# Performance work log

Measured on AMD Instinct MI355X. Metric: run time of the kernel, lower is better.

The kernel has to match this reference:

```python
import jax, jax.numpy as jnp
import numpy as np

N_NODES = 100000


def setup_inputs() -> dict:
    key = jax.random.key(0)
    ks = jax.random.split(key, 8)
    IN, HID, OUT = 128, 128, 64
    E = 1600000
    x = jax.random.normal(ks[0], (N_NODES, IN), dtype=jnp.float32)
    edge_index = jax.random.randint(ks[1], (2, E), 0, N_NODES, dtype=jnp.int64)
    # PyG SAGEConv params: lin_l (applied to aggregated neighbors, with bias),
    # lin_r (root weight, no bias).
    def lin(k, fi, fo):
        return jax.random.normal(k, (fi, fo), dtype=jnp.float32) / np.sqrt(fi)
    Wl0 = lin(ks[2], IN, HID)
    bl0 = jnp.zeros((HID,), dtype=jnp.float32)
    Wr0 = lin(ks[3], IN, HID)
    Wl1 = lin(ks[4], HID, OUT)
    bl1 = jnp.zeros((OUT,), dtype=jnp.float32)
    Wr1 = lin(ks[5], HID, OUT)
    return {"x": x, "edge_index": edge_index,
            "Wl0": Wl0, "bl0": bl0, "Wr0": Wr0,
            "Wl1": Wl1, "bl1": bl1, "Wr1": Wr1}


def _sage_conv(h, src, dst, Wl, bl, Wr):
    # mean aggregation of source features onto target nodes
    summed = jax.ops.segment_sum(h[src], dst, num_segments=N_NODES)  # [N, d]
    cnt = jax.ops.segment_sum(jnp.ones((src.shape[0], 1), h.dtype), dst,
                              num_segments=N_NODES)                  # [N, 1]
    agg = summed / jnp.maximum(cnt, 1.0)
    return agg @ Wl + bl + h @ Wr


def reference(x, edge_index, Wl0, bl0, Wr0, Wl1, bl1, Wr1):
    src, dst = edge_index[0], edge_index[1]
    h = jax.nn.relu(_sage_conv(x, src, dst, Wl0, bl0, Wr0))
    # dropout is identity in eval mode (training=False)
    return _sage_conv(h, src, dst, Wl1, bl1, Wr1)
```

## Files before the change

### kernel.cpp

```cpp
#include <hip/hip_runtime.h>


typedef short short8 __attribute__((ext_vector_type(8)));
typedef float f32x4 __attribute__((ext_vector_type(4)));
typedef float f32x2 __attribute__((ext_vector_type(2)));

#define NBUCK 782
#define BCAP  3072
#define EPB   8192

static __device__ __forceinline__ unsigned short f2bf(float f) {
    union { float f; unsigned u; } c; c.f = f;
    unsigned u = c.u + 0x7fffu + ((c.u >> 16) & 1u);
    return (unsigned short)(u >> 16);
}
static __device__ __forceinline__ float bf2f(unsigned short b) {
    union { unsigned u; float f; } c; c.u = ((unsigned)b) << 16;
    return c.f;
}
static __device__ __forceinline__ float bf2f_s(short b) {
    return bf2f((unsigned short)b);
}

static __device__ __forceinline__ unsigned char f2fp8(float x) {
    union { float f; unsigned u; } c; c.f = x;
    unsigned s = (c.u >> 24) & 0x80u;
    float a = __builtin_fabsf(x);
    if (a < 0.015625f) {
        int m = (int)rintf(a * 512.0f);
        return (unsigned char)(s | (unsigned)m);
    }
    unsigned u = c.u + 0x7ffffu + ((c.u >> 20) & 1u);
    int e = (int)((u >> 23) & 0xff) - 120;
    unsigned m = (u >> 20) & 7u;
    if (e > 15) { e = 15; m = 6; }
    return (unsigned char)(s | (unsigned)(e << 3) | m);
}

static __device__ __forceinline__ void acc_fp8x4(unsigned w, float* a) {
#if __has_builtin(__builtin_amdgcn_cvt_pk_f32_fp8)
    f32x2 lo = __builtin_amdgcn_cvt_pk_f32_fp8((int)w, false);
    f32x2 hi = __builtin_amdgcn_cvt_pk_f32_fp8((int)w, true);
    a[0] += lo[0]; a[1] += lo[1]; a[2] += hi[0]; a[3] += hi[1];
#else
    #pragma unroll
    for (int j = 0; j < 4; ++j) {
        unsigned b = (w >> (8 * j)) & 0xffu;
        union { unsigned u; float f; } c;
        c.u = ((b & 0x80u) << 24) | ((b & 0x7fu) << 20);
        a[j] += c.f * 0x1p120f;
    }
#endif
}
static __device__ __forceinline__ void acc_row16(uint4 w, float* a) {
    acc_fp8x4(w.x, a + 0);  acc_fp8x4(w.y, a + 4);
    acc_fp8x4(w.z, a + 8);  acc_fp8x4(w.w, a + 12);
}

__global__ __launch_bounds__(256) void k_pack2(const float* __restrict__ Wl0,
        const float* __restrict__ Wr0, const float* __restrict__ Wl1,
        const float* __restrict__ Wr1, unsigned short* __restrict__ Wp0,
        unsigned short* __restrict__ Wp1) {
    int tid = blockIdx.x * 256 + threadIdx.x;
    const float *WA, *WB; int CA; unsigned short* Wp;
    if (tid < 4096) {
        WA = Wl0; WB = Wr0; CA = 128; Wp = Wp0;
    } else {
        tid -= 4096;
        if (tid >= 2048) return;
        WA = Wl1; WB = Wr1; CA = 64; Wp = Wp1;
    }
    int lane = tid & 63, kk = (tid >> 6) & 3, tg = tid >> 8;
    int l15 = lane & 15, quad = lane >> 4;
    int c = tg * 16 + l15;
    const float* W = (c < CA) ? WA : WB;
    int cc = (c < CA) ? c : c - CA;
    short8 v;
    #pragma unroll
    for (int j = 0; j < 8; ++j) {
        int k = kk * 32 + quad * 8 + j;
        v[j] = (short)f2bf(W[(size_t)k * CA + cc]);
    }
    *(short8*)(Wp + (size_t)tid * 8) = v;
}

__global__ __launch_bounds__(512) void k_gemm0_bucket(
        const float* __restrict__ X, const unsigned short* __restrict__ Wp,
        unsigned char* __restrict__ P0, unsigned short* __restrict__ Q0, int Nrows,
        const int* __restrict__ src, const int* __restrict__ dst,
        int* __restrict__ cursor, int* __restrict__ bregion,
        int E, int bucketBlocks) {
    const int t = threadIdx.x;
    if ((int)blockIdx.x >= bucketBlocks) {
        const int wave = t >> 6, lane = t & 63;
        const int sub = wave >> 2, wv = wave & 3;
        const int quad = lane >> 4, l15 = lane & 15;
        const int row0 = (blockIdx.x - bucketBlocks) * 64 + sub * 32;
        const int c0w = wv * 64;
        float4 xf[4][2][2];
        #pragma unroll
        for (int mt = 0; mt < 2; ++mt) {
            int row = row0 + mt * 16 + l15;
            if (row > Nrows - 1) row = Nrows - 1;
            const float* xp = X + (size_t)row * 128 + quad * 8;
            #pragma unroll
            for (int kk = 0; kk < 4; ++kk) {
                xf[kk][mt][0] = *(const float4*)(xp + kk * 32);
                xf[kk][mt][1] = *(const float4*)(xp + kk * 32 + 4);
            }
        }
        short8 a[4][2];
        #pragma unroll
        for (int kk = 0; kk < 4; ++kk)
            #pragma unroll
            for (int mt = 0; mt < 2; ++mt) {
                float4 f0 = xf[kk][mt][0], f1 = xf[kk][mt][1];
                short8 v;
                v[0] = (short)f2bf(f0.x); v[1] = (short)f2bf(f0.y);
                v[2] = (short)f2bf(f0.z); v[3] = (short)f2bf(f0.w);
                v[4] = (short)f2bf(f1.x); v[5] = (short)f2bf(f1.y);
                v[6] = (short)f2bf(f1.z); v[7] = (short)f2bf(f1.w);
                a[kk][mt] = v;
            }
        f32x4 acc[2][4];
        #pragma unroll
        for (int mt = 0; mt < 2; ++mt)
            #pragma unroll
            for (int tt = 0; tt < 4; ++tt) acc[mt][tt] = (f32x4){0.f, 0.f, 0.f, 0.f};
        #pragma unroll
        for (int kk = 0; kk < 4; ++kk) {
            short8 b[4];
            #pragma unroll
            for (int tt = 0; tt < 4; ++tt) {
                int tg = (c0w >> 4) + tt;
                b[tt] = *(const short8*)(Wp + ((size_t)(tg * 4 + kk) * 64 + lane) * 8);
            }
            #pragma unroll
            for (int mt = 0; mt < 2; ++mt)
                #pragma unroll
                for (int tt = 0; tt < 4; ++tt)
                    acc[mt][tt] = __builtin_amdgcn_mfma_f32_16x16x32_bf16(
                        a[kk][mt], b[tt], acc[mt][tt], 0, 0, 0);
        }
        #pragma unroll
        for (int mt = 0; mt < 2; ++mt)
            #pragma unroll
            for (int r = 0; r < 4; ++r) {
                int row = row0 + mt * 16 + quad * 4 + r;
                if (row < Nrows) {
                    if (c0w < 128) {
                        #pragma unroll
                        for (int tt = 0; tt < 4; ++tt)
                            P0[(size_t)row * 128 + c0w + tt * 16 + l15] =
                                f2fp8(acc[mt][tt][r]);
                    } else {
                        #pragma unroll
                        for (int tt = 0; tt < 4; ++tt)
                            Q0[(size_t)row * 128 + (c0w - 128) + tt * 16 + l15] =
                                f2bf(acc[mt][tt][r]);
                    }
                }
            }
        return;
    }
    __shared__ int hist[NBUCK];
    __shared__ int basel[NBUCK];
    int bid = blockIdx.x;
    for (int i = t; i < NBUCK; i += 512) hist[i] = 0;
    __syncthreads();
    int e0 = bid * EPB + t * 16;
    if (e0 + 16 <= E) {
        #pragma unroll
        for (int q = 0; q < 4; ++q) {
            int4 v = *(const int4*)(dst + e0 + q * 4);
            atomicAdd(&hist[v.x >> 7], 1);
            atomicAdd(&hist[v.y >> 7], 1);
            atomicAdd(&hist[v.z >> 7], 1);
            atomicAdd(&hist[v.w >> 7], 1);
        }
    } else {
        for (int j = 0; j < 16; ++j)
            if (e0 + j < E) atomicAdd(&hist[dst[e0 + j] >> 7], 1);
    }
    __syncthreads();
    for (int i = t; i < NBUCK; i += 512) {
        int c = hist[i];
        basel[i] = (c > 0) ? atomicAdd(&cursor[i], c) : 0;
    }
    __syncthreads();
    for (int i = t; i < NBUCK; i += 512) hist[i] = 0;
    __syncthreads();
    if (e0 + 16 <= E) {
        #pragma unroll
        for (int q = 0; q < 4; ++q) {
            int4 dv = *(const int4*)(dst + e0 + q * 4);
            int4 sv = *(const int4*)(src + e0 + q * 4);
            int dd[4] = {dv.x, dv.y, dv.z, dv.w};
            int ss[4] = {sv.x, sv.y, sv.z, sv.w};
            #pragma unroll
            for (int j = 0; j < 4; ++j) {
                int b = dd[j] >> 7;
                int r = atomicAdd(&hist[b], 1);
                bregion[(size_t)b * BCAP + basel[b] + r] = ss[j] | ((dd[j] & 127) << 20);
            }
        }
    } else {
        for (int j = 0; j < 16; ++j) {
            if (e0 + j < E) {
                int dd = dst[e0 + j], ss = src[e0 + j];
                int b = dd >> 7;
                int r = atomicAdd(&hist[b], 1);
                bregion[(size_t)b * BCAP + basel[b] + r] = ss | ((dd & 127) << 20);
            }
        }
    }
}

__global__ __launch_bounds__(256) void k_csr(const int* __restrict__ cursor,
                                             const int* __restrict__ bregion,
                                             int* __restrict__ rowptr,
                                             int* __restrict__ csr, int Nn) {
    __shared__ int words[BCAP];
    __shared__ int hist[1024], sc[1024], rank[1024];
    __shared__ int red[256];
    int b = blockIdx.x, t = threadIdx.x;
    int part = 0;
    for (int i = t; i < b; i += 256) part += cursor[i];
    red[t] = part;
    for (int i = t; i < 1024; i += 256) { hist[i] = 0; rank[i] = 0; }
    __syncthreads();
    #pragma unroll
    for (int off = 128; off > 0; off >>= 1) {
        if (t < off) red[t] += red[t + off];
        __syncthreads();
    }
    int gbase = red[0];
    __syncthreads();
    int cnt = cursor[b];
    for (int i = t; i < cnt; i += 256) {
        int w = bregion[(size_t)b * BCAP + i];
        words[i] = w;
        int key = ((w >> 20) << 3) | ((w & 0xFFFFF) >> 14);
        atomicAdd(&hist[key], 1);
    }
    __syncthreads();
    int i0 = t * 4;
    int h0 = hist[i0], h1 = hist[i0 + 1], h2 = hist[i0 + 2], h3 = hist[i0 + 3];
    int lsum = h0 + h1 + h2 + h3;
    red[t] = lsum;
    __syncthreads();
    #pragma unroll
    for (int off = 1; off < 256; off <<= 1) {
        int x = (t >= off) ? red[t - off] : 0;
        __syncthreads();
        red[t] += x;
        __syncthreads();
    }
    int excl = red[t] - lsum;
    sc[i0]     = excl;
    sc[i0 + 1] = excl + h0;
    sc[i0 + 2] = excl + h0 + h1;
    sc[i0 + 3] = excl + h0 + h1 + h2;
    __syncthreads();
    if (t < 128) {
        int node = b * 128 + t;
        if (node <= Nn) rowptr[node] = gbase + sc[t << 3];
    }
    for (int i = t; i < cnt; i += 256) {
        int w = words[i];
        int key = ((w >> 20) << 3) | ((w & 0xFFFFF) >> 14);
        int r = atomicAdd(&rank[key], 1);
        csr[gbase + sc[key] + r] = w & 0xFFFFF;
    }
}

__global__ __launch_bounds__(256) void k_agg0_gemm1(
        const unsigned char* __restrict__ P0,
        const unsigned short* __restrict__ Q0,
        const int* __restrict__ rowptr, const int* __restrict__ csr,
        const float* __restrict__ bl0,
        const unsigned short* __restrict__ Wp,
        unsigned char* __restrict__ P1, unsigned short* __restrict__ Q1,
        int Nn) {
    __shared__ unsigned short ht[32 * 128];
    const int t = threadIdx.x;
    const int wave = t >> 6, lane = t & 63;
    {
        int g = lane >> 3, l7 = lane & 7;
        int nloc = wave * 8 + g;
        int n = blockIdx.x * 32 + nloc;
        bool live = (n < Nn);
        int st = 0, dg = 0;
        if (live) { st = rowptr[n]; dg = rowptr[n + 1] - st; }
        float acc[16] = {};
        int e = 0;
        for (; e + 4 <= dg; e += 4) {
            int s0 = csr[st + e];
            int s1 = csr[st + e + 1];
            int s2 = csr[st + e + 2];
            int s3 = csr[st + e + 3];
            uint4 w0 = *(const uint4*)(P0 + (size_t)s0 * 128 + l7 * 16);
            uint4 w1 = *(const uint4*)(P0 + (size_t)s1 * 128 + l7 * 16);
            uint4 w2 = *(const uint4*)(P0 + (size_t)s2 * 128 + l7 * 16);
            uint4 w3 = *(const uint4*)(P0 + (size_t)s3 * 128 + l7 * 16);
            acc_row16(w0, acc);
            acc_row16(w1, acc);
            acc_row16(w2, acc);
            acc_row16(w3, acc);
        }
        for (; e < dg; ++e) {
            int s0 = csr[st + e];
            uint4 w0 = *(const uint4*)(P0 + (size_t)s0 * 128 + l7 * 16);
            acc_row16(w0, acc);
        }
        short8 o0 = (short8){0,0,0,0,0,0,0,0}, o1 = o0;
        if (live) {
            float inv = 1.f / fmaxf((float)dg, 1.f);
            short8 q0 = *(const short8*)(Q0 + (size_t)n * 128 + l7 * 16);
            short8 q1 = *(const short8*)(Q0 + (size_t)n * 128 + l7 * 16 + 8);
            float bb[16];
            *(float4*)(bb + 0)  = *(const float4*)(bl0 + l7 * 16);
            *(float4*)(bb + 4)  = *(const float4*)(bl0 + l7 * 16 + 4);
            *(float4*)(bb + 8)  = *(const float4*)(bl0 + l7 * 16 + 8);
            *(float4*)(bb + 12) = *(const float4*)(bl0 + l7 * 16 + 12);
            #pragma unroll
            for (int j = 0; j < 8; ++j)
                o0[j] = (short)f2bf(fmaxf(acc[j] * inv + bb[j] + bf2f_s(q0[j]), 0.f));
            #pragma unroll
            for (int j = 0; j < 8; ++j)
                o1[j] = (short)f2bf(fmaxf(acc[8 + j] * inv + bb[8 + j] + bf2f_s(q1[j]), 0.f));
        }
        unsigned sw = (unsigned)(nloc & 7) << 4;
        char* base = (char*)ht + nloc * 256;
        *(short8*)(base + (((unsigned)(l7 * 32)) ^ sw)) = o0;
        *(short8*)(base + (((unsigned)(l7 * 32 + 16)) ^ sw)) = o1;
    }
    __syncthreads();
    const int quad = lane >> 4, l15 = lane & 15;
    const int row0 = blockIdx.x * 32;
    const int c0w = wave * 32;
    f32x4 acc[2][2];
    #pragma unroll
    for (int mt = 0; mt < 2; ++mt)
        #pragma unroll
        for (int tt = 0; tt < 2; ++tt) acc[mt][tt] = (f32x4){0.f, 0.f, 0.f, 0.f};
    #pragma unroll
    for (int kk = 0; kk < 4; ++kk) {
        short8 a[2];
        #pragma unroll
        for (int mt = 0; mt < 2; ++mt) {
            int row = mt * 16 + l15;
            const char* p = (const char*)ht + row * 256 +
                (((unsigned)(kk * 64 + quad * 16)) ^ ((unsigned)(row & 7) << 4));
            a[mt] = *(const short8*)p;
        }
        short8 b[2];
        #pragma unroll
        for (int tt = 0; tt < 2; ++tt) {
            int tg = (c0w >> 4) + tt;
            b[tt] = *(const short8*)(Wp + ((size_t)(tg * 4 + kk) * 64 + lane) * 8);
        }
        #pragma unroll
        for (int mt = 0; mt < 2; ++mt)
            #pragma unroll
            for (int tt = 0; tt < 2; ++tt)
                acc[mt][tt] = __builtin_amdgcn_mfma_f32_16x16x32_bf16(
                    a[mt], b[tt], acc[mt][tt], 0, 0, 0);
    }
    #pragma unroll
    for (int mt = 0; mt < 2; ++mt)
        #pragma unroll
        for (int r = 0; r < 4; ++r) {
            int row = row0 + mt * 16 + quad * 4 + r;
            if (row < Nn) {
                if (c0w < 64) {
                    #pragma unroll
                    for (int tt = 0; tt < 2; ++tt)
                        P1[(size_t)row * 64 + c0w + tt * 16 + l15] =
                            f2fp8(acc[mt][tt][r]);
                } else {
                    #pragma unroll
                    for (int tt = 0; tt < 2; ++tt)
                        Q1[(size_t)row * 64 + (c0w - 64) + tt * 16 + l15] =
                            f2bf(acc[mt][tt][r]);
                }
            }
        }
}

__global__ __launch_bounds__(256) void k_agg1(const unsigned char* __restrict__ P1,
                                              const unsigned short* __restrict__ Q1,
                                              const int* __restrict__ rowptr,
                                              const int* __restrict__ csr,
                                              const float* __restrict__ bl1,
                                              float* __restrict__ out, int Nn) {
    int wave = threadIdx.x >> 6, lane = threadIdx.x & 63;
    int g = lane >> 2, l3 = lane & 3;
    int n = (blockIdx.x * 4 + wave) * 16 + g;
    bool live = (n < Nn);
    int st = 0, dg = 0;
    if (live) { st = rowptr[n]; dg = rowptr[n + 1] - st; }
    float acc[16] = {};
    int e = 0;
    for (; e + 4 <= dg; e += 4) {
        int s0 = csr[st + e];
        int s1 = csr[st + e + 1];
        int s2 = csr[st + e + 2];
        int s3 = csr[st + e + 3];
        uint4 w0 = *(const uint4*)(P1 + (size_t)s0 * 64 + l3 * 16);
        uint4 w1 = *(const uint4*)(P1 + (size_t)s1 * 64 + l3 * 16);
        uint4 w2 = *(const uint4*)(P1 + (size_t)s2 * 64 + l3 * 16);
        uint4 w3 = *(const uint4*)(P1 + (size_t)s3 * 64 + l3 * 16);
        acc_row16(w0, acc);
        acc_row16(w1, acc);
        acc_row16(w2, acc);
        acc_row16(w3, acc);
    }
    for (; e < dg; ++e) {
        int s0 = csr[st + e];
        uint4 w0 = *(const uint4*)(P1 + (size_t)s0 * 64 + l3 * 16);
        acc_row16(w0, acc);
    }
    if (live) {
        float inv = 1.f / fmaxf((float)dg, 1.f);
        short8 q0 = *(const short8*)(Q1 + (size_t)n * 64 + l3 * 16);
        short8 q1 = *(const short8*)(Q1 + (size_t)n * 64 + l3 * 16 + 8);
        float bb[16];
        *(float4*)(bb + 0)  = *(const float4*)(bl1 + l3 * 16);
        *(float4*)(bb + 4)  = *(const float4*)(bl1 + l3 * 16 + 4);
        *(float4*)(bb + 8)  = *(const float4*)(bl1 + l3 * 16 + 8);
        *(float4*)(bb + 12) = *(const float4*)(bl1 + l3 * 16 + 12);
        float4 o[4];
        #pragma unroll
        for (int j = 0; j < 8; ++j)
            ((float*)o)[j] = acc[j] * inv + bb[j] + bf2f_s(q0[j]);
        #pragma unroll
        for (int j = 0; j < 8; ++j)
            ((float*)o)[8 + j] = acc[8 + j] * inv + bb[8 + j] + bf2f_s(q1[j]);
        #pragma unroll
        for (int q = 0; q < 4; ++q)
            *(float4*)(out + (size_t)n * 64 + l3 * 16 + q * 4) = o[q];
    }
}

extern "C" void kernel_launch(void* const* d_in, const int* in_sizes, int n_in,
                              void* d_out, int out_size, void* d_ws, size_t ws_size,
                              hipStream_t stream) {
    const float* x   = (const float*)d_in[0];
    const int* eidx  = (const int*)d_in[1];
    const float* Wl0 = (const float*)d_in[2];
    const float* bl0 = (const float*)d_in[3];
    const float* Wr0 = (const float*)d_in[4];
    const float* Wl1 = (const float*)d_in[5];
    const float* bl1 = (const float*)d_in[6];
    const float* Wr1 = (const float*)d_in[7];
    float* out = (float*)d_out;

    const int N = in_sizes[0] / 128;
    const int E = in_sizes[1] / 2;
    const int* src = eidx;
    const int* dst = eidx + E;

    int* rowptr  = (int*)d_ws;
    int* cursor  = rowptr + (N + 4);
    int* bregion = cursor + 784;
    int* csr     = bregion + (size_t)NBUCK * BCAP;
    unsigned short* Wp0 = (unsigned short*)(csr + E);
    unsigned short* Wp1 = Wp0 + 32768;
    unsigned char*  P0  = (unsigned char*)(Wp1 + 16384);
    unsigned short* Q0  = (unsigned short*)(P0 + (size_t)N * 128);
    unsigned char*  P1  = (unsigned char*)(Q0 + (size_t)N * 128);
    unsigned short* Q1  = (unsigned short*)(P1 + (size_t)N * 64);

    hipMemsetAsync(cursor, 0, NBUCK * sizeof(int), stream);

    k_pack2<<<24, 256, 0, stream>>>(Wl0, Wr0, Wl1, Wr1, Wp0, Wp1);

    int gemmBlocks = (N + 63) / 64;
    int nbb = (E + EPB - 1) / EPB;
    k_gemm0_bucket<<<gemmBlocks + nbb, 512, 0, stream>>>(
        x, Wp0, P0, Q0, N, src, dst, cursor, bregion, E, nbb);
    k_csr<<<NBUCK, 256, 0, stream>>>(cursor, bregion, rowptr, csr, N);

    k_agg0_gemm1<<<(N + 31) / 32, 256, 0, stream>>>(
        P0, Q0, rowptr, csr, bl0, Wp1, P1, Q1, N);
    k_agg1<<<(N + 63) / 64, 256, 0, stream>>>(P1, Q1, rowptr, csr, bl1, out, N);
}
```

Before: 272.2 us.

## Fuse CSR build into gemm0/bucket kernel with a spin-wait counter

```diff
diff --git a/kernel.cpp b/kernel.cpp
--- a/kernel.cpp
+++ b/kernel.cpp
@@ -89,13 +89,16 @@
         unsigned char* __restrict__ P0, unsigned short* __restrict__ Q0, int Nrows,
         const int* __restrict__ src, const int* __restrict__ dst,
         int* __restrict__ cursor, int* __restrict__ bregion,
-        int E, int bucketBlocks) {
+        int* __restrict__ rowptr, int* __restrict__ csr,
+        int E, int bucketBlocks, int gemmBlocks) {
+    __shared__ int sh[6656];
     const int t = threadIdx.x;
-    if ((int)blockIdx.x >= bucketBlocks) {
+    const int bid = blockIdx.x;
+    if (bid >= bucketBlocks && bid < bucketBlocks + gemmBlocks) {
         const int wave = t >> 6, lane = t & 63;
         const int sub = wave >> 2, wv = wave & 3;
         const int quad = lane >> 4, l15 = lane & 15;
-        const int row0 = (blockIdx.x - bucketBlocks) * 64 + sub * 32;
+        const int row0 = (bid - bucketBlocks) * 64 + sub * 32;
         const int c0w = wv * 64;
         float4 xf[4][2][2];
         #pragma unroll
@@ -163,114 +166,123 @@
             }
         return;
     }
-    __shared__ int hist[NBUCK];
-    __shared__ int basel[NBUCK];
-    int bid = blockIdx.x;
-    for (int i = t; i < NBUCK; i += 512) hist[i] = 0;
+    if (bid < bucketBlocks) {
+        int* hist  = sh;
+        int* basel = sh + NBUCK;
+        for (int i = t; i < NBUCK; i += 512) hist[i] = 0;
+        __syncthreads();
+        int e0 = bid * EPB + t * 16;
+        if (e0 + 16 <= E) {
+            #pragma unroll
+            for (int q = 0; q < 4; ++q) {
+                int4 v = *(const int4*)(dst + e0 + q * 4);
+                atomicAdd(&hist[v.x >> 7], 1);
+                atomicAdd(&hist[v.y >> 7], 1);
+                atomicAdd(&hist[v.z >> 7], 1);
+                atomicAdd(&hist[v.w >> 7], 1);
+            }
+        } else {
+            for (int j = 0; j < 16; ++j)
+                if (e0 + j < E) atomicAdd(&hist[dst[e0 + j] >> 7], 1);
+        }
+        __syncthreads();
+        for (int i = t; i < NBUCK; i += 512) {
+            int c = hist[i];
+            basel[i] = (c > 0) ? atomicAdd(&cursor[i], c) : 0;
+        }
+        __syncthreads();
+        for (int i = t; i < NBUCK; i += 512) hist[i] = 0;
+        __syncthreads();
+        if (e0 + 16 <= E) {
+            #pragma unroll
+            for (int q = 0; q < 4; ++q) {
+                int4 dv = *(const int4*)(dst + e0 + q * 4);
+                int4 sv = *(const int4*)(src + e0 + q * 4);
+                int dd[4] = {dv.x, dv.y, dv.z, dv.w};
+                int ss[4] = {sv.x, sv.y, sv.z, sv.w};
+                #pragma unroll
+                for (int j = 0; j < 4; ++j) {
+                    int b = dd[j] >> 7;
+                    int r = atomicAdd(&hist[b], 1);
+                    bregion[(size_t)b * BCAP + basel[b] + r] = ss[j] | ((dd[j] & 127) << 20);
+                }
+            }
+        } else {
+            for (int j = 0; j < 16; ++j) {
+                if (e0 + j < E) {
+                    int dd = dst[e0 + j], ss = src[e0 + j];
+                    int b = dd >> 7;
+                    int r = atomicAdd(&hist[b], 1);
+                    bregion[(size_t)b * BCAP + basel[b] + r] = ss | ((dd & 127) << 20);
+                }
+            }
+        }
+        __threadfence();
+        __syncthreads();
+        if (t == 0) atomicAdd(&cursor[782], 1);
+        return;
+    }
+    int cb = bid - bucketBlocks - gemmBlocks;
+    if (t == 0) {
+        while (atomicAdd(&cursor[782], 0) < bucketBlocks)
+            __builtin_amdgcn_s_sleep(8);
+    }
     __syncthreads();
-    int e0 = bid * EPB + t * 16;
-    if (e0 + 16 <= E) {
-        #pragma unroll
-        for (int q = 0; q < 4; ++q) {
-            int4 v = *(const int4*)(dst + e0 + q * 4);
-            atomicAdd(&hist[v.x >> 7], 1);
-            atomicAdd(&hist[v.y >> 7], 1);
-            atomicAdd(&hist[v.z >> 7], 1);
-            atomicAdd(&hist[v.w >> 7], 1);
-        }
-    } else {
-        for (int j = 0; j < 16; ++j)
-            if (e0 + j < E) atomicAdd(&hist[dst[e0 + j] >> 7], 1);
-    }
-    __syncthreads();
-    for (int i = t; i < NBUCK; i += 512) {
-        int c = hist[i];
-        basel[i] = (c > 0) ? atomicAdd(&cursor[i], c) : 0;
-    }
-    __syncthreads();
-    for (int i = t; i < NBUCK; i += 512) hist[i] = 0;
-    __syncthreads();
-    if (e0 + 16 <= E) {
-        #pragma unroll
-        for (int q = 0; q < 4; ++q) {
-            int4 dv = *(const int4*)(dst + e0 + q * 4);
-            int4 sv = *(const int4*)(src + e0 + q * 4);
-            int dd[4] = {dv.x, dv.y, dv.z, dv.w};
-            int ss[4] = {sv.x, sv.y, sv.z, sv.w};
-            #pragma unroll
-            for (int j = 0; j < 4; ++j) {
-                int b = dd[j] >> 7;
-                int r = atomicAdd(&hist[b], 1);
-                bregion[(size_t)b * BCAP + basel[b] + r] = ss[j] | ((dd[j] & 127) << 20);
-            }
-        }
-    } else {
-        for (int j = 0; j < 16; ++j) {
-            if (e0 + j < E) {
-                int dd = dst[e0 + j], ss = src[e0 + j];
-                int b = dd >> 7;
-                int r = atomicAdd(&hist[b], 1);
-                bregion[(size_t)b * BCAP + basel[b] + r] = ss | ((dd & 127) << 20);
-            }
-        }
-    }
-}
-
-__global__ __launch_bounds__(256) void k_csr(const int* __restrict__ cursor,
-                                             const int* __restrict__ bregion,
-                                             int* __restrict__ rowptr,
-                                             int* __restrict__ csr, int Nn) {
-    __shared__ int words[BCAP];
-    __shared__ int hist[1024], sc[1024], rank[1024];
-    __shared__ int red[256];
-    int b = blockIdx.x, t = threadIdx.x;
-    int part = 0;
-    for (int i = t; i < b; i += 256) part += cursor[i];
-    red[t] = part;
-    for (int i = t; i < 1024; i += 256) { hist[i] = 0; rank[i] = 0; }
-    __syncthreads();
-    #pragma unroll
-    for (int off = 128; off > 0; off >>= 1) {
-        if (t < off) red[t] += red[t + off];
-        __syncthreads();
-    }
-    int gbase = red[0];
-    __syncthreads();
-    int cnt = cursor[b];
-    for (int i = t; i < cnt; i += 256) {
-        int w = bregion[(size_t)b * BCAP + i];
-        words[i] = w;
-        int key = ((w >> 20) << 3) | ((w & 0xFFFFF) >> 14);
-        atomicAdd(&hist[key], 1);
-    }
-    __syncthreads();
-    int i0 = t * 4;
-    int h0 = hist[i0], h1 = hist[i0 + 1], h2 = hist[i0 + 2], h3 = hist[i0 + 3];
-    int lsum = h0 + h1 + h2 + h3;
-    red[t] = lsum;
-    __syncthreads();
-    #pragma unroll
-    for (int off = 1; off < 256; off <<= 1) {
-        int x = (t >= off) ? red[t - off] : 0;
-        __syncthreads();
-        red[t] += x;
-        __syncthreads();
-    }
-    int excl = red[t] - lsum;
-    sc[i0]     = excl;
-    sc[i0 + 1] = excl + h0;
-    sc[i0 + 2] = excl + h0 + h1;
-    sc[i0 + 3] = excl + h0 + h1 + h2;
-    __syncthreads();
-    if (t < 128) {
-        int node = b * 128 + t;
-        if (node <= Nn) rowptr[node] = gbase + sc[t << 3];
-    }
-    for (int i = t; i < cnt; i += 256) {
-        int w = words[i];
-        int key = ((w >> 20) << 3) | ((w & 0xFFFFF) >> 14);
-        int r = atomicAdd(&rank[key], 1);
-        csr[gbase + sc[key] + r] = w & 0xFFFFF;
+    __threadfence();
+    int* words = sh;
+    int* hist  = sh + 3072;
+    int* sc    = sh + 4096;
+    int* rank  = sh + 5120;
+    int* red   = sh + 6144;
+    for (int half = 0; half < 2; ++half) {
+        int b = cb * 2 + half;
+        int part = 0;
+        for (int i = t; i < b; i += 512) part += cursor[i];
+        red[t] = part;
+        for (int i = t; i < 1024; i += 512) { hist[i] = 0; rank[i] = 0; }
+        __syncthreads();
+        #pragma unroll
+        for (int off = 256; off > 0; off >>= 1) {
+            if (t < off) red[t] += red[t + off];
+            __syncthreads();
+        }
+        int gbase = red[0];
+        __syncthreads();
+        int cnt = cursor[b];
+        for (int i = t; i < cnt; i += 512) {
+            int w = bregion[(size_t)b * BCAP + i];
+            words[i] = w;
+            int key = ((w >> 20) << 3) | ((w & 0xFFFFF) >> 14);
+            atomicAdd(&hist[key], 1);
+        }
+        __syncthreads();
+        int i0 = t * 2;
+        int h0 = hist[i0], h1 = hist[i0 + 1];
+        int lsum = h0 + h1;
+        red[t] = lsum;
+        __syncthreads();
+        #pragma unroll
+        for (int off = 1; off < 512; off <<= 1) {
+            int x = (t >= off) ? red[t - off] : 0;
+            __syncthreads();
+            red[t] += x;
+            __syncthreads();
+        }
+        int excl = red[t] - lsum;
+        sc[i0]     = excl;
+        sc[i0 + 1] = excl + h0;
+        __syncthreads();
+        if (t < 128) {
+            int node = b * 128 + t;
+            if (node <= Nrows) rowptr[node] = gbase + sc[t << 3];
+        }
+        for (int i = t; i < cnt; i += 512) {
+            int w = words[i];
+            int key = ((w >> 20) << 3) | ((w & 0xFFFFF) >> 14);
+            int r = atomicAdd(&rank[key], 1);
+            csr[gbase + sc[key] + r] = w & 0xFFFFF;
+        }
+        __syncthreads();
     }
 }
 
@@ -472,15 +484,16 @@
     unsigned char*  P1  = (unsigned char*)(Q0 + (size_t)N * 128);
     unsigned short* Q1  = (unsigned short*)(P1 + (size_t)N * 64);
 
-    hipMemsetAsync(cursor, 0, NBUCK * sizeof(int), stream);
+    hipMemsetAsync(cursor, 0, 784 * sizeof(int), stream);
 
     k_pack2<<<24, 256, 0, stream>>>(Wl0, Wr0, Wl1, Wr1, Wp0, Wp1);
 
     int gemmBlocks = (N + 63) / 64;
     int nbb = (E + EPB - 1) / EPB;
-    k_gemm0_bucket<<<gemmBlocks + nbb, 512, 0, stream>>>(
-        x, Wp0, P0, Q0, N, src, dst, cursor, bregion, E, nbb);
-    k_csr<<<NBUCK, 256, 0, stream>>>(cursor, bregion, rowptr, csr, N);
+    int csrBlocks = NBUCK / 2;
+    k_gemm0_bucket<<<nbb + gemmBlocks + csrBlocks, 512, 0, stream>>>(
+        x, Wp0, P0, Q0, N, src, dst, cursor, bregion, rowptr, csr,
+        E, nbb, gemmBlocks);
 
     k_agg0_gemm1<<<(N + 31) / 32, 256, 0, stream>>>(
         P0, Q0, rowptr, csr, bl0, Wp1, P1, Q1, N);
```

After: 466.9 us. 71.5% more time.
